# Kernel tuning notes

Hardware: AMD Instinct MI355X
Metric: run time of the kernel (lower is better)

Reference implementation:

```python
import jax, jax.numpy as jnp
import numpy as np


def setup_inputs() -> dict:
    key = jax.random.key(0)
    k1, k2 = jax.random.split(key)
    embeddings = jax.random.normal(k1, (32, 512, 1024), dtype=jnp.float32)
    aspect = jax.random.normal(k2, (32, 1024), dtype=jnp.float32)
    return {"embeddings": embeddings, "aspect": aspect}


def reference(embeddings, aspect):
    # go_backwards=False, so no sequence reversal.
    # L2-normalize embeddings per token and aspect per sample.
    e = embeddings / jnp.linalg.norm(embeddings, axis=2, keepdims=True)
    a = aspect / jnp.linalg.norm(aspect, axis=1, keepdims=True)
    # NaN-mask (zero-norm rows produce NaN after division).
    e = jnp.where(jnp.isnan(e), jnp.zeros_like(e), e)
    a = jnp.where(jnp.isnan(a), jnp.zeros_like(a), a)
    # Circulant matrix: circ[b, i, j] = a[b, (j - i) mod D]
    # (matches the TF scatter_nd construction M[i, (i+k)%D] = a[k]).
    D = e.shape[-1]
    r = jnp.arange(D)
    idx = (r[None, :] - r[:, None]) % D  # [D, D]
    circ = a[:, idx]  # [B, D, D]
    # matmul(e, circ, transpose_b=True): out[b,s,i] = sum_j e[b,s,j] * circ[b,i,j]
    return jnp.einsum('bsd,bid->bsi', e, circ)
```

## Files before the change

### kernel.cpp

```cpp
#include <hip/hip_runtime.h>
#include <hip/hip_bf16.h>

typedef __attribute__((ext_vector_type(8))) short bf16x8;
typedef __attribute__((ext_vector_type(4))) float f32x4;
typedef __attribute__((ext_vector_type(4))) unsigned int u32x4;

#define NB 32
#define NS 512
#define ND 1024

__device__ __forceinline__ unsigned short f2bf(float f) {
  unsigned int u = __float_as_uint(f);
  u = (u + 0x7FFFu + ((u >> 16) & 1u)) >> 16;
  return (unsigned short)u;
}

__global__ void anorm_kernel(const float* __restrict__ aspect,
                             unsigned short* __restrict__ a_n) {
  int b = blockIdx.x;
  int t = threadIdx.x;
  const float4* p = (const float4*)(aspect + (size_t)b * ND);
  float4 v = p[t];
  float s = v.x * v.x + v.y * v.y + v.z * v.z + v.w * v.w;
#pragma unroll
  for (int off = 32; off >= 1; off >>= 1) s += __shfl_down(s, off);
  __shared__ float red[4];
  if ((t & 63) == 0) red[t >> 6] = s;
  __syncthreads();
  float tot = red[0] + red[1] + red[2] + red[3];
  float inv = (tot > 0.f) ? (1.f / sqrtf(tot)) : 0.f;
  ushort4 u;
  u.x = f2bf(v.x * inv); u.y = f2bf(v.y * inv);
  u.z = f2bf(v.z * inv); u.w = f2bf(v.w * inv);
  ((ushort4*)(a_n + (size_t)b * ND))[t] = u;
}

__global__ __launch_bounds__(256, 2)
void corr_gemm11_kernel(const float* __restrict__ emb,
                        const unsigned short* __restrict__ a_n,
                        float* __restrict__ out) {
  __shared__ __align__(16) unsigned short Abuf[2][128][64];
  __shared__ __align__(16) unsigned short copies[8 * 1288];
  __shared__ float invnLDS[128];

  const int b = blockIdx.x, mt = blockIdx.y, nt = blockIdx.z;
  const int n0 = nt * 256, m0 = mt * 128;
  const int tid = threadIdx.x;

  const int lane = tid & 63, wn = tid >> 6;
  const int q = lane >> 4, l16 = lane & 15;
  const int mx = l16 & 7;
  const int s00 = (q ^ mx) * 8;
  const int s01 = ((4 + q) ^ mx) * 8;

  const int pB = (8 - mx) & 7;
  const unsigned short* Bp = copies + pB * 1287 + (256 + 8 * q - wn * 64 - l16);

  const int r0 = tid >> 3, cw = tid & 7;
  const int sw = cw ^ (r0 & 7);
  const float* gA = emb + ((size_t)b * NS + m0 + r0) * ND + cw * 8;

  unsigned short av[40];
  {
    const unsigned short* an = a_n + (size_t)b * ND;
    const int p = tid & 7;
    const int x0 = (tid >> 3) * 40;
    const int base = (768 - n0 + p) & 1023;
#pragma unroll
    for (int j = 0; j < 40; ++j) av[j] = an[(base + x0 + j) & 1023];
  }

  float4 g[8];
  float ss0 = 0.f, ss1 = 0.f, ss2 = 0.f, ss3 = 0.f;

#define LOADG(KTT)                                                       \
  do {                                                                   \
    _Pragma("unroll")                                                    \
    for (int j = 0; j < 4; ++j) {                                        \
      const float* _p = gA + (size_t)j * 32 * ND + (KTT) * 64;           \
      g[2 * j] = *(const float4*)_p;                                     \
      g[2 * j + 1] = *(const float4*)(_p + 4);                           \
    }                                                                    \
  } while (0)

#define CVT_WRITE(NBUF)                                                  \
  do {                                                                   \
    _Pragma("unroll")                                                    \
    for (int j = 0; j < 4; ++j) {                                        \
      float4 va = g[2 * j], vb = g[2 * j + 1];                           \
      float _s = va.x * va.x + va.y * va.y + va.z * va.z + va.w * va.w   \
               + vb.x * vb.x + vb.y * vb.y + vb.z * vb.z + vb.w * vb.w;  \
      if (j == 0) ss0 += _s; else if (j == 1) ss1 += _s;                 \
      else if (j == 2) ss2 += _s; else ss3 += _s;                        \
      u32x4 w;                                                           \
      w[0] = (unsigned)f2bf(va.x) | ((unsigned)f2bf(va.y) << 16);        \
      w[1] = (unsigned)f2bf(va.z) | ((unsigned)f2bf(va.w) << 16);        \
      w[2] = (unsigned)f2bf(vb.x) | ((unsigned)f2bf(vb.y) << 16);        \
      w[3] = (unsigned)f2bf(vb.z) | ((unsigned)f2bf(vb.w) << 16);       \
      *(u32x4*)&Abuf[NBUF][r0 + 32 * j][sw * 8] = w;                     \
    }                                                                    \
  } while (0)

  LOADG(0);
  {
    const int p = tid & 7;
    const int x0 = (tid >> 3) * 40;
#pragma unroll
    for (int j = 0; j < 40; ++j) copies[p * 1288 + x0 + j] = av[j];
  }
  CVT_WRITE(0);
  LOADG(1);
  __syncthreads();

  f32x4 acc[8][4];
#pragma unroll
  for (int i = 0; i < 8; ++i)
#pragma unroll
    for (int j = 0; j < 4; ++j)
      acc[i][j] = (f32x4){0.f, 0.f, 0.f, 0.f};

  bf16x8 a0[4], a1[4], bfr[4][2];

#define ISSUE_A(DST, BASE, PHN)                                             \
  do {                                                                      \
    DST[0] = *(const bf16x8*)&(BASE)[(PHN) * 32 + l16][s00];                \
    DST[1] = *(const bf16x8*)&(BASE)[(PHN) * 32 + l16][s01];                \
    DST[2] = *(const bf16x8*)&(BASE)[(PHN) * 32 + 16 + l16][s00];           \
    DST[3] = *(const bf16x8*)&(BASE)[(PHN) * 32 + 16 + l16][s01];           \
  } while (0)

#define LOAD_B(KTT)                                                 \
  do {                                                              \
    const unsigned short* Bt = Bp + (KTT) * 64;                     \
    _Pragma("unroll")                                               \
    for (int n = 0; n < 4; ++n) {                                   \
      bfr[n][0] = *(const bf16x8*)(Bt - n * 16);                    \
      bfr[n][1] = *(const bf16x8*)(Bt + 32 - n * 16);               \
    }                                                               \
  } while (0)

#define MFMA_PH(PH, CS)                                                                       \
  do {                                                                                        \
    __builtin_amdgcn_s_setprio(1);                                                            \
    _Pragma("unroll")                                                                         \
    for (int n = 0; n < 4; ++n) {                                                             \
      acc[2*(PH)][n]   = __builtin_amdgcn_mfma_f32_16x16x32_bf16(CS[0], bfr[n][0], acc[2*(PH)][n],   0, 0, 0); \
      acc[2*(PH)][n]   = __builtin_amdgcn_mfma_f32_16x16x32_bf16(CS[1], bfr[n][1], acc[2*(PH)][n],   0, 0, 0); \
      acc[2*(PH)+1][n] = __builtin_amdgcn_mfma_f32_16x16x32_bf16(CS[2], bfr[n][0], acc[2*(PH)+1][n], 0, 0, 0); \
      acc[2*(PH)+1][n] = __builtin_amdgcn_mfma_f32_16x16x32_bf16(CS[3], bfr[n][1], acc[2*(PH)+1][n], 0, 0, 0); \
    }                                                                                         \
    __builtin_amdgcn_s_setprio(0);                                                            \
  } while (0)

#pragma unroll 1
  for (int kt = 0; kt < 16; ++kt) {
    const unsigned short (*At)[64] = Abuf[kt & 1];

    ISSUE_A(a0, At, 0);
    LOAD_B(kt);
    ISSUE_A(a1, At, 1);
    asm volatile("s_waitcnt lgkmcnt(4)" ::: "memory");
    __builtin_amdgcn_sched_barrier(0);
    MFMA_PH(0, a0);

    ISSUE_A(a0, At, 2);
    asm volatile("s_waitcnt lgkmcnt(4)" ::: "memory");
    __builtin_amdgcn_sched_barrier(0);
    MFMA_PH(1, a1);

    ISSUE_A(a1, At, 3);
    asm volatile("s_waitcnt lgkmcnt(4)" ::: "memory");
    __builtin_amdgcn_sched_barrier(0);
    MFMA_PH(2, a0);

    asm volatile("s_waitcnt lgkmcnt(0)" ::: "memory");
    __builtin_amdgcn_sched_barrier(0);
    MFMA_PH(3, a1);

    if (kt < 15) {
      asm volatile("s_waitcnt vmcnt(0)" ::: "memory");
      __builtin_amdgcn_sched_barrier(0);
      CVT_WRITE((kt & 1) ^ 1);
      if (kt < 14) LOADG(kt + 2);
      asm volatile("s_waitcnt lgkmcnt(0)" ::: "memory");
      __builtin_amdgcn_sched_barrier(0);
    }
    __builtin_amdgcn_s_barrier();
  }
#undef MFMA_PH
#undef LOAD_B
#undef ISSUE_A

#pragma unroll
  for (int off = 4; off >= 1; off >>= 1) {
    ss0 += __shfl_xor(ss0, off);
    ss1 += __shfl_xor(ss1, off);
    ss2 += __shfl_xor(ss2, off);
    ss3 += __shfl_xor(ss3, off);
  }
  if ((lane & 7) == 0) {
    invnLDS[r0 +  0] = (ss0 > 0.f) ? (1.f / sqrtf(ss0)) : 0.f;
    invnLDS[r0 + 32] = (ss1 > 0.f) ? (1.f / sqrtf(ss1)) : 0.f;
    invnLDS[r0 + 64] = (ss2 > 0.f) ? (1.f / sqrtf(ss2)) : 0.f;
    invnLDS[r0 + 96] = (ss3 > 0.f) ? (1.f / sqrtf(ss3)) : 0.f;
  }
  __syncthreads();

  float* outB = out + ((size_t)b * NS + m0) * ND + n0;
#pragma unroll
  for (int i = 0; i < 8; ++i) {
    f32x4 iv = *(const f32x4*)&invnLDS[i * 16 + q * 4];
#pragma unroll
    for (int rg = 0; rg < 4; ++rg) {
      int r = i * 16 + q * 4 + rg;
      float* orow = outB + (size_t)r * ND + wn * 64 + l16;
#pragma unroll
      for (int n = 0; n < 4; ++n)
        orow[n * 16] = acc[i][n][rg] * iv[rg];
    }
  }
#undef CVT_WRITE
#undef LOADG
}

__global__ void enorm_kernel(const float* __restrict__ emb,
                             float* __restrict__ inv_norm) {
  int wave = threadIdx.x >> 6;
  int lane = threadIdx.x & 63;
  int row = blockIdx.x * 4 + wave;
  const float4* p = (const float4*)(emb + (size_t)row * ND);
  float s = 0.f;
#pragma unroll
  for (int j = 0; j < 4; ++j) {
    float4 v = p[lane + 64 * j];
    s += v.x * v.x + v.y * v.y + v.z * v.z + v.w * v.w;
  }
#pragma unroll
  for (int off = 32; off >= 1; off >>= 1) s += __shfl_down(s, off);
  if (lane == 0) inv_norm[row] = (s > 0.f) ? (1.f / sqrtf(s)) : 0.f;
}

__global__ __launch_bounds__(256)
void corr_gemm_kernel(const float* __restrict__ emb,
                      const float* __restrict__ inv_norm,
                      const unsigned short* __restrict__ a_n,
                      float* __restrict__ out) {
  __shared__ unsigned short copies[8][2056];
  __shared__ unsigned short Atile[128][40];

  const int nt = blockIdx.x, mt = blockIdx.y, b = blockIdx.z;
  const int n0 = nt * 128, m0 = mt * 128;
  const int t = threadIdx.x;

  {
    const unsigned short* an = a_n + (size_t)b * ND;
    int p = t & 7;
    int x0 = (t >> 3) * 64;
#pragma unroll
    for (int j = 0; j < 64; j += 4) {
      ushort4 u;
      u.x = an[(x0 + j + 0 + p) & 1023];
      u.y = an[(x0 + j + 1 + p) & 1023];
      u.z = an[(x0 + j + 2 + p) & 1023];
      u.w = an[(x0 + j + 3 + p) & 1023];
      *(ushort4*)&copies[p][x0 + j] = u;
    }
  }

  const int ar = t >> 3;
  const int ac = (t & 7) * 4;
  float invn[4];
#pragma unroll
  for (int w = 0; w < 4; ++w)
    invn[w] = inv_norm[b * NS + m0 + ar + 32 * w];

  const int lane = t & 63;
  const int wv = t >> 6;
  const int wm = wv >> 1, wn = wv & 1;
  const int q = lane >> 4, l16 = lane & 15;

  f32x4 acc[4][4];
#pragma unroll
  for (int i = 0; i < 4; ++i)
#pragma unroll
    for (int j = 0; j < 4; ++j)
      acc[i][j] = (f32x4){0.f, 0.f, 0.f, 0.f};

  const float* embB = emb + ((size_t)b * NS + m0) * ND;

  for (int k0 = 0; k0 < ND; k0 += 32) {
    __syncthreads();
#pragma unroll
    for (int w = 0; w < 4; ++w) {
      int r = ar + 32 * w;
      float4 v = *(const float4*)(embB + (size_t)r * ND + k0 + ac);
      float in = invn[w];
      ushort4 u;
      u.x = f2bf(v.x * in); u.y = f2bf(v.y * in);
      u.z = f2bf(v.z * in); u.w = f2bf(v.w * in);
      *(ushort4*)&Atile[r][ac] = u;
    }
    __syncthreads();

    bf16x8 af[4], bfr[4];
#pragma unroll
    for (int r = 0; r < 4; ++r) {
      int m = wm * 64 + r * 16 + l16;
      af[r] = *(const bf16x8*)&Atile[m][q * 8];
    }
#pragma unroll
    for (int r = 0; r < 4; ++r) {
      int ng = n0 + wn * 64 + r * 16 + l16;
      int e0 = k0 + 8 * q - ng + 1024;
      int p = e0 & 7;
      bfr[r] = *(const bf16x8*)&copies[p][e0 - p];
    }
#pragma unroll
    for (int i = 0; i < 4; ++i)
#pragma unroll
      for (int j = 0; j < 4; ++j)
        acc[i][j] = __builtin_amdgcn_mfma_f32_16x16x32_bf16(af[i], bfr[j], acc[i][j], 0, 0, 0);
  }

  float* outB = out + ((size_t)b * NS + m0) * ND + n0;
#pragma unroll
  for (int i = 0; i < 4; ++i) {
#pragma unroll
    for (int rg = 0; rg < 4; ++rg) {
      int s = wm * 64 + i * 16 + q * 4 + rg;
      float* orow = outB + (size_t)s * ND + wn * 64 + l16;
#pragma unroll
      for (int j = 0; j < 4; ++j)
        orow[j * 16] = acc[i][j][rg];
    }
  }
}

extern "C" void kernel_launch(void* const* d_in, const int* in_sizes, int n_in,
                              void* d_out, int out_size, void* d_ws, size_t ws_size,
                              hipStream_t stream) {
  const float* emb = (const float*)d_in[0];
  const float* aspect = (const float*)d_in[1];
  float* out = (float*)d_out;

  if (ws_size >= 65536) {
    unsigned short* a_n = (unsigned short*)d_ws;
    anorm_kernel<<<NB, 256, 0, stream>>>(aspect, a_n);
    corr_gemm11_kernel<<<dim3(NB, 4, 4), 256, 0, stream>>>(emb, a_n, out);
  } else {
    float* inv_norm = (float*)d_ws;
    unsigned short* a_n = (unsigned short*)((char*)d_ws + 65536);
    enorm_kernel<<<4096, 256, 0, stream>>>(emb, inv_norm);
    anorm_kernel<<<NB, 256, 0, stream>>>(aspect, a_n);
    corr_gemm_kernel<<<dim3(8, 4, NB), 256, 0, stream>>>(emb, inv_norm, a_n, out);
  }
}
```

Before: 138.6 us.

## Interleave fp32-to-bf16 conversion of next tile between MFMA phases

Splits the per-tile conversion and LDS write of the next embedding tile into four row-group chunks and places each chunk between MFMA phases. Fine-grained vmcnt waits then let global loads drain progressively instead of all at once after the math. The last k-tile is peeled out of the loop so the loop body needs no branch. It also switches to packed hardware bf16 conversion. The hand-tuned waitcnt counts must match the issued load and LDS ops exactly, otherwise results are wrong.

```diff
diff --git a/kernel.cpp b/kernel.cpp
--- a/kernel.cpp
+++ b/kernel.cpp
@@ -13,6 +13,13 @@
   unsigned int u = __float_as_uint(f);
   u = (u + 0x7FFFu + ((u >> 16) & 1u)) >> 16;
   return (unsigned short)u;
+}
+
+__device__ __forceinline__ unsigned int pkbf(float lo, float hi) {
+  __hip_bfloat162 h = __float22bfloat162_rn(make_float2(lo, hi));
+  union { __hip_bfloat162 h2; unsigned int u; } cv;
+  cv.h2 = h;
+  return cv.u;
 }
 
 __global__ void anorm_kernel(const float* __restrict__ aspect,
@@ -36,7 +43,7 @@
 }
 
 __global__ __launch_bounds__(256, 2)
-void corr_gemm11_kernel(const float* __restrict__ emb,
+void corr_gemm12_kernel(const float* __restrict__ emb,
                         const unsigned short* __restrict__ a_n,
                         float* __restrict__ out) {
   __shared__ __align__(16) unsigned short Abuf[2][128][64];
@@ -80,25 +87,21 @@
       const float* _p = gA + (size_t)j * 32 * ND + (KTT) * 64;           \
       g[2 * j] = *(const float4*)_p;                                     \
       g[2 * j + 1] = *(const float4*)(_p + 4);                           \
+      __builtin_amdgcn_sched_barrier(0);   \
     }                                                                    \
   } while (0)
 
-#define CVT_WRITE(NBUF)                                                  \
+#define CVT_J(NBUF, J, SS)                                               \
   do {                                                                   \
-    _Pragma("unroll")                                                    \
-    for (int j = 0; j < 4; ++j) {                                        \
-      float4 va = g[2 * j], vb = g[2 * j + 1];                           \
-      float _s = va.x * va.x + va.y * va.y + va.z * va.z + va.w * va.w   \
-               + vb.x * vb.x + vb.y * vb.y + vb.z * vb.z + vb.w * vb.w;  \
-      if (j == 0) ss0 += _s; else if (j == 1) ss1 += _s;                 \
-      else if (j == 2) ss2 += _s; else ss3 += _s;                        \
-      u32x4 w;                                                           \
-      w[0] = (unsigned)f2bf(va.x) | ((unsigned)f2bf(va.y) << 16);        \
-      w[1] = (unsigned)f2bf(va.z) | ((unsigned)f2bf(va.w) << 16);        \
-      w[2] = (unsigned)f2bf(vb.x) | ((unsigned)f2bf(vb.y) << 16);        \
-      w[3] = (unsigned)f2bf(vb.z) | ((unsigned)f2bf(vb.w) << 16);       \
-      *(u32x4*)&Abuf[NBUF][r0 + 32 * j][sw * 8] = w;                     \
-    }                                                                    \
+    float4 va = g[2 * (J)], vb = g[2 * (J) + 1];                         \
+    SS += va.x * va.x + va.y * va.y + va.z * va.z + va.w * va.w          \
+        + vb.x * vb.x + vb.y * vb.y + vb.z * vb.z + vb.w * vb.w;         \
+    u32x4 w;                                                             \
+    w[0] = pkbf(va.x, va.y);                                             \
+    w[1] = pkbf(va.z, va.w);                                             \
+    w[2] = pkbf(vb.x, vb.y);                                             \
+    w[3] = pkbf(vb.z, vb.w);                                             \
+    *(u32x4*)&Abuf[NBUF][r0 + 32 * (J)][sw * 8] = w;                     \
   } while (0)
 
   LOADG(0);
@@ -108,7 +111,7 @@
 #pragma unroll
     for (int j = 0; j < 40; ++j) copies[p * 1288 + x0 + j] = av[j];
   }
-  CVT_WRITE(0);
+  CVT_J(0, 0, ss0); CVT_J(0, 1, ss1); CVT_J(0, 2, ss2); CVT_J(0, 3, ss3);
   LOADG(1);
   __syncthreads();
 
@@ -153,39 +156,70 @@
   } while (0)
 
 #pragma unroll 1
-  for (int kt = 0; kt < 16; ++kt) {
+  for (int kt = 0; kt < 15; ++kt) {
     const unsigned short (*At)[64] = Abuf[kt & 1];
+    const int nb = (kt & 1) ^ 1;
 
     ISSUE_A(a0, At, 0);
     LOAD_B(kt);
+    __builtin_amdgcn_sched_barrier(0);
     ISSUE_A(a1, At, 1);
     asm volatile("s_waitcnt lgkmcnt(4)" ::: "memory");
     __builtin_amdgcn_sched_barrier(0);
     MFMA_PH(0, a0);
 
+    asm volatile("s_waitcnt vmcnt(6)" ::: "memory");
+    __builtin_amdgcn_sched_barrier(0);
+    CVT_J(nb, 0, ss0);
+    ISSUE_A(a0, At, 2);
+    asm volatile("s_waitcnt lgkmcnt(5)" ::: "memory");
+    __builtin_amdgcn_sched_barrier(0);
+    MFMA_PH(1, a1);
+
+    asm volatile("s_waitcnt vmcnt(4)" ::: "memory");
+    __builtin_amdgcn_sched_barrier(0);
+    CVT_J(nb, 1, ss1);
+    ISSUE_A(a1, At, 3);
+    asm volatile("s_waitcnt lgkmcnt(5)" ::: "memory");
+    __builtin_amdgcn_sched_barrier(0);
+    MFMA_PH(2, a0);
+
+    asm volatile("s_waitcnt vmcnt(2)" ::: "memory");
+    __builtin_amdgcn_sched_barrier(0);
+    CVT_J(nb, 2, ss2);
+    asm volatile("s_waitcnt lgkmcnt(1)" ::: "memory");
+    __builtin_amdgcn_sched_barrier(0);
+    MFMA_PH(3, a1);
+
+    asm volatile("s_waitcnt vmcnt(0)" ::: "memory");
+    __builtin_amdgcn_sched_barrier(0);
+    CVT_J(nb, 3, ss3);
+    if (kt < 14) LOADG(kt + 2);
+    asm volatile("s_waitcnt lgkmcnt(0)" ::: "memory");
+    __builtin_amdgcn_sched_barrier(0);
+    __builtin_amdgcn_s_barrier();
+  }
+
+  {
+    const unsigned short (*At)[64] = Abuf[1];
+    ISSUE_A(a0, At, 0);
+    LOAD_B(15);
+    __builtin_amdgcn_sched_barrier(0);
+    ISSUE_A(a1, At, 1);
+    asm volatile("s_waitcnt lgkmcnt(4)" ::: "memory");
+    __builtin_amdgcn_sched_barrier(0);
+    MFMA_PH(0, a0);
     ISSUE_A(a0, At, 2);
     asm volatile("s_waitcnt lgkmcnt(4)" ::: "memory");
     __builtin_amdgcn_sched_barrier(0);
     MFMA_PH(1, a1);
-
     ISSUE_A(a1, At, 3);
     asm volatile("s_waitcnt lgkmcnt(4)" ::: "memory");
     __builtin_amdgcn_sched_barrier(0);
     MFMA_PH(2, a0);
-
     asm volatile("s_waitcnt lgkmcnt(0)" ::: "memory");
     __builtin_amdgcn_sched_barrier(0);
     MFMA_PH(3, a1);
-
-    if (kt < 15) {
-      asm volatile("s_waitcnt vmcnt(0)" ::: "memory");
-      __builtin_amdgcn_sched_barrier(0);
-      CVT_WRITE((kt & 1) ^ 1);
-      if (kt < 14) LOADG(kt + 2);
-      asm volatile("s_waitcnt lgkmcnt(0)" ::: "memory");
-      __builtin_amdgcn_sched_barrier(0);
-    }
-    __builtin_amdgcn_s_barrier();
   }
 #undef MFMA_PH
 #undef LOAD_B
@@ -219,7 +253,7 @@
         orow[n * 16] = acc[i][n][rg] * iv[rg];
     }
   }
-#undef CVT_WRITE
+#undef CVT_J
 #undef LOADG
 }
 
@@ -346,7 +380,7 @@
   if (ws_size >= 65536) {
     unsigned short* a_n = (unsigned short*)d_ws;
     anorm_kernel<<<NB, 256, 0, stream>>>(aspect, a_n);
-    corr_gemm11_kernel<<<dim3(NB, 4, 4), 256, 0, stream>>>(emb, a_n, out);
+    corr_gemm12_kernel<<<dim3(NB, 4, 4), 256, 0, stream>>>(emb, a_n, out);
   } else {
     float* inv_norm = (float*)d_ws;
     unsigned short* a_n = (unsigned short*)((char*)d_ws + 65536);
```

New measurement: 157.1 us. +13.3%, slower.
